# Performance work log

Hardware: AMD Instinct MI355X
Metric: run time of the kernel (lower is better)

## Reference

```python
import jax, jax.numpy as jnp
import numpy as np

BN_EPS = 1e-5

def _bn_train(x, g, b):
    # BatchNorm1d in training mode: biased batch stats over the row dim
    m = x.mean(0)
    v = x.var(0)
    return g * (x - m) * jax.lax.rsqrt(v + BN_EPS) + b


def setup_inputs() -> dict:
    key = jax.random.key(0)
    ks = jax.random.split(key, 16)
    N, V, C, H, T, NC, OD, EH, EC = 128, 128, 256, 512, 12, 5, 5, 256, 256
    s = 0.05
    idx = jax.random.randint(ks[1], (T, N), 0, NC)
    return {
        "x": jax.random.normal(ks[0], (N, V, C), jnp.float32),
        "hidden_states": jnp.zeros((N, V, H), jnp.float32),
        "cell_states": jnp.zeros((N, V, H), jnp.float32),
        "one_hots_c_pred_seq": jax.nn.one_hot(idx, NC, dtype=jnp.float32),
        "W_ih": jax.random.normal(ks[2], (4 * H, C), jnp.float32) * s,
        "W_hh": jax.random.normal(ks[3], (4 * H, H), jnp.float32) * s,
        "b_ih": jax.random.normal(ks[4], (4 * H,), jnp.float32) * s,
        "b_hh": jax.random.normal(ks[5], (4 * H,), jnp.float32) * s,
        "W_cls": jax.random.normal(ks[6], (NC, H), jnp.float32) * s,
        "b_cls": jax.random.normal(ks[7], (NC,), jnp.float32) * s,
        "W_eh": jax.random.normal(ks[8], (EH, H), jnp.float32) * s,
        "b_eh": jax.random.normal(ks[9], (EH,), jnp.float32) * s,
        "g_eh": jnp.ones((EH,), jnp.float32),
        "beta_eh": jnp.zeros((EH,), jnp.float32),
        "W_ec": jax.random.normal(ks[10], (EC, NC), jnp.float32) * s,
        "b_ec": jax.random.normal(ks[11], (EC,), jnp.float32) * s,
        "g_ec": jnp.ones((EC,), jnp.float32),
        "beta_ec": jnp.zeros((EC,), jnp.float32),
        "W_out": jax.random.normal(ks[12], (OD, EH + EC), jnp.float32) * s,
        "b_out": jax.random.normal(ks[13], (OD,), jnp.float32) * s,
    }


def reference(x, hidden_states, cell_states, one_hots_c_pred_seq,
              W_ih, W_hh, b_ih, b_hh, W_cls, b_cls,
              W_eh, b_eh, g_eh, beta_eh, W_ec, b_ec, g_ec, beta_ec,
              W_out, b_out):
    N, V, C = x.shape
    H = hidden_states.shape[-1]
    xf = x.reshape(N * V, C)
    gx = xf @ W_ih.T + b_ih  # input gates are identical every step (x is repeated)

    def step(carry, onehot):
        h, c = carry  # [N*V, H]
        gates = gx + h @ W_hh.T + b_hh
        i, f, g, o = jnp.split(gates, 4, axis=1)  # pytorch LSTMCell gate order
        c = jax.nn.sigmoid(f) * c + jax.nn.sigmoid(i) * jnp.tanh(g)
        h = jax.nn.sigmoid(o) * jnp.tanh(c)
        # ClassifierLayer: avg-pool over V then 1x1 conv == mean + linear
        oc = h.reshape(N, V, H).mean(1) @ W_cls.T + b_cls  # [N, nc]
        # PredictionLayer
        eh = jax.nn.relu(_bn_train(h @ W_eh.T + b_eh, g_eh, beta_eh))
        ohr = jnp.broadcast_to(onehot[:, None, :], (N, V, onehot.shape[-1])).reshape(N * V, -1)
        ec = jax.nn.relu(_bn_train(ohr @ W_ec.T + b_ec, g_ec, beta_ec))
        op = jnp.concatenate([eh, ec], axis=1) @ W_out.T + b_out  # [N*V, out_dim]
        return (h, c), (op.reshape(N, V, -1), oc)

    carry0 = (hidden_states.reshape(N * V, H), cell_states.reshape(N * V, H))
    _, (preds, c_outs) = jax.lax.scan(step, carry0, one_hots_c_pred_seq)
    preds = preds.transpose(1, 0, 2, 3)  # [N, T, V, out_dim]
    # output_activation: bivariate-Gaussian params
    pred_outs = jnp.stack([preds[..., 0], preds[..., 1],
                           jnp.exp(preds[..., 2]), jnp.exp(preds[..., 3]),
                           jnp.tanh(preds[..., 4])], axis=-1)
    return pred_outs, c_outs
```

## Files before the change

kernel.cpp:

```cpp
#include <hip/hip_runtime.h>
#include <hip/hip_bf16.h>
#include <stdint.h>

typedef __hip_bfloat16 bf16;
typedef __attribute__((ext_vector_type(8))) short bf16x8;
typedef __attribute__((ext_vector_type(4))) short bf16x4;
typedef __attribute__((ext_vector_type(4))) float f32x4;

#define NN 128
#define VV 128
#define CC 256
#define HH 512
#define TT 12
#define NCLS 5
#define OD 5
#define EHD 256
#define KCAT (HH + CC)
#define ROWS (NN * VV)
#define PRED_SZ (NN * TT * VV * OD)
#define LDP 72
#define MiB (1ull << 20)


__device__ __forceinline__ float sigm(float x) { return 1.f / (1.f + __expf(-x)); }
__device__ __forceinline__ float tanh_(float x) {
    x = fminf(fmaxf(x, -15.f), 15.f);
    float e = __expf(2.f * x);
    return (e - 1.f) / (e + 1.f);
}
__device__ __forceinline__ float bf2f(unsigned short v) {
    unsigned u = ((unsigned)v) << 16; float f; __builtin_memcpy(&f, &u, 4); return f;
}
__device__ __forceinline__ float ldin(const void* p, int i, int is32) {
    return is32 ? ((const float*)p)[i] : __bfloat162float(((const bf16*)p)[i]);
}

__global__ void detect_dtype(const void* g_eh, int* flag, int* hnz) {
    unsigned w = *(const unsigned*)g_eh;
    *flag = (w == 0x3F800000u) ? 1 : 0;
    *hnz = 0;
}

__global__ __launch_bounds__(256) void convert_in(const void* src, bf16* dst, int n, const int* flag) {
    int is32 = *flag;
    int i = blockIdx.x * 256 + threadIdx.x;
    int stride = gridDim.x * 256;
    if (is32) { const float* s = (const float*)src; for (; i < n; i += stride) dst[i] = __float2bfloat16(s[i]); }
    else      { const bf16*  s = (const bf16*)src;  for (; i < n; i += stride) dst[i] = s[i]; }
}

__global__ __launch_bounds__(256) void convert_in_hflag(const void* src, bf16* dst, int n, const int* flag,
                                                        int* nz) {
    int is32 = *flag;
    int i = blockIdx.x * 256 + threadIdx.x;
    int stride = gridDim.x * 256;
    int loc = 0;
    if (is32) {
        const float* s = (const float*)src;
        for (; i < n; i += stride) { float v = s[i]; if (__float_as_uint(v) != 0u) loc = 1; dst[i] = __float2bfloat16(v); }
    } else {
        const bf16* s = (const bf16*)src;
        for (; i < n; i += stride) { bf16 v = s[i]; if (*(const unsigned short*)&v) loc = 1; dst[i] = v; }
    }
    if (loc) atomicOr(nz, 1);
}

__global__ __launch_bounds__(256) void init_c(const void* cell, bf16* c, const int* flag) {
    int is32 = *flag;
    size_t i = (size_t)blockIdx.x * 256 + threadIdx.x;
    const size_t total = (size_t)ROWS * HH;
    for (; i < total; i += (size_t)8192 * 256) c[i] = __float2bfloat16(ldin(cell, (int)i, is32));
}

__device__ __forceinline__ void issue_loads(const bf16* __restrict__ A, int lda, int row0, int ka,
                                            const bf16* __restrict__ B, int ldb, int col0, int kb,
                                            bf16x8 ar[4], bf16x8 br[4]) {
    int tid = threadIdx.x;
#pragma unroll
    for (int it = 0; it < 4; ++it) {
        int cidx = tid + 256 * it;
        int row = cidx >> 3;
        int cc8 = (cidx & 7) * 8;
        ar[it] = *(const bf16x8*)(A + (size_t)(row0 + row) * lda + ka + cc8);
        br[it] = *(const bf16x8*)(B + (size_t)(col0 + row) * ldb + kb + cc8);
    }
}
__device__ __forceinline__ void write_lds(bf16* As, bf16* Bs, const bf16x8 ar[4], const bf16x8 br[4]) {
    int tid = threadIdx.x;
#pragma unroll
    for (int it = 0; it < 4; ++it) {
        int cidx = tid + 256 * it;
        int row = cidx >> 3;
        int cc8 = (cidx & 7) * 8;
        *(bf16x8*)(As + row * LDP + cc8) = ar[it];
        *(bf16x8*)(Bs + row * LDP + cc8) = br[it];
    }
}

__device__ __forceinline__ void tile_mfma(const bf16* As, const bf16* Bs, f32x4 acc[4][4]) {
    const int lane = threadIdx.x & 63, wave = threadIdx.x >> 6;
    const int wro = (wave >> 1) * 64, wco = (wave & 1) * 64;
    const int l15 = lane & 15, l8 = (lane >> 4) * 8;
#pragma unroll
    for (int kk = 0; kk < 64; kk += 32) {
        bf16x8 af[4], bg[4];
#pragma unroll
        for (int x = 0; x < 4; ++x) {
            af[x] = *(const bf16x8*)(As + (wro + x * 16 + l15) * LDP + kk + l8);
            bg[x] = *(const bf16x8*)(Bs + (wco + x * 16 + l15) * LDP + kk + l8);
        }
#pragma unroll
        for (int bi = 0; bi < 4; ++bi)
#pragma unroll
            for (int bj = 0; bj < 4; ++bj)
                acc[bi][bj] = __builtin_amdgcn_mfma_f32_16x16x32_bf16(af[bi], bg[bj], acc[bi][bj], 0, 0, 0);
    }
}

__global__ __launch_bounds__(256) void prep_weights(const void* __restrict__ Wih, const void* __restrict__ Whh,
                                                    const void* __restrict__ bih, const void* __restrict__ bhh,
                                                    bf16* __restrict__ Wihp, bf16* __restrict__ Whhp,
                                                    float* __restrict__ biasp, const int* flag) {
    int is32 = *flag;
    int jg = blockIdx.x;
    int b = jg >> 7, j = jg & 127;
    int gate = (j >> 4) & 3;
    int unit = b * 32 + (j & 15) + 16 * (j >> 6);
    int p = gate * HH + unit;
    for (int k = threadIdx.x; k < HH; k += 256)
        Whhp[(size_t)jg * HH + k] = __float2bfloat16(ldin(Whh, p * HH + k, is32));
    for (int k = threadIdx.x; k < CC; k += 256)
        Wihp[(size_t)jg * CC + k] = __float2bfloat16(ldin(Wih, p * CC + k, is32));
    if (threadIdx.x == 0)
        biasp[jg] = ldin(bih, p, is32) + ldin(bhh, p, is32);
}

__global__ __launch_bounds__(256) void gemm_k0(const bf16* __restrict__ A, const bf16* __restrict__ B,
                                               const float* __restrict__ biasp, bf16* __restrict__ gx) {
    __shared__ bf16 As[128 * LDP], Bs[128 * LDP];
    f32x4 acc[4][4] = {};
    bf16x8 ar[4], br[4];
    int row0 = blockIdx.x * 128, col0 = blockIdx.y * 128;
    issue_loads(A, CC, row0, 0, B, CC, col0, 0, ar, br);
    for (int k0 = 0; k0 < CC; k0 += 64) {
        __syncthreads();
        write_lds(As, Bs, ar, br);
        __syncthreads();
        int kn = k0 + 64;
        if (kn < CC) issue_loads(A, CC, row0, kn, B, CC, col0, kn, ar, br);
        tile_mfma(As, Bs, acc);
    }
    int lane = threadIdx.x & 63, wave = threadIdx.x >> 6;
    int wro = (wave >> 1) * 64, wco = (wave & 1) * 64;
    int l15 = lane & 15, lr4 = (lane >> 4) * 4;
#pragma unroll
    for (int bj = 0; bj < 4; ++bj) {
        int j = wco + bj * 16 + l15;
        float bia = biasp[col0 + j];
        int sidx = wco + l15 * 4 + bj;
#pragma unroll
        for (int bi = 0; bi < 4; ++bi)
#pragma unroll
            for (int reg = 0; reg < 4; ++reg) {
                int r = row0 + wro + bi * 16 + lr4 + reg;
                gx[(size_t)r * 2048 + col0 + sidx] = __float2bfloat16(acc[bi][bj][reg] + bia);
            }
    }
}

__global__ __launch_bounds__(256) void ec_precompute(const void* __restrict__ W_ec, const void* __restrict__ b_ec,
                                                     const void* __restrict__ g_ec, const void* __restrict__ beta_ec,
                                                     const void* __restrict__ W_out, const void* __restrict__ b_out,
                                                     const void* __restrict__ onehot, float* __restrict__ ecd_all,
                                                     const int* flag) {
    __shared__ float ecv[NCLS][EHD];
    __shared__ float cntf[NCLS];
    __shared__ float ecdc[NCLS][OD];
    int is32 = *flag;
    int t = blockIdx.x, tid = threadIdx.x;
    int ohoff = t * NN * NCLS;
    if (tid < NCLS) {
        float cnum = 0.f;
        for (int n = 0; n < NN; ++n) cnum += ldin(onehot, ohoff + n * NCLS + tid, is32);
        cntf[tid] = cnum * (1.f / NN);
    }
    __syncthreads();
    {
        int j = tid;
        float vals[NCLS];
        float m = 0.f, e2 = 0.f;
        float be = ldin(b_ec, j, is32);
        for (int cc = 0; cc < NCLS; ++cc) {
            vals[cc] = ldin(W_ec, j * NCLS + cc, is32) + be;
            m += cntf[cc] * vals[cc];
            e2 += cntf[cc] * vals[cc] * vals[cc];
        }
        float rs = rsqrtf(e2 - m * m + 1e-5f);
        float g = ldin(g_ec, j, is32), bt = ldin(beta_ec, j, is32);
        for (int cc = 0; cc < NCLS; ++cc)
            ecv[cc][j] = fmaxf(g * (vals[cc] - m) * rs + bt, 0.f);
    }
    __syncthreads();
    if (tid < NCLS * OD) {
        int cc = tid / OD, k = tid % OD;
        float s = 0.f;
        for (int j = 0; j < EHD; ++j) s += ecv[cc][j] * ldin(W_out, k * (EHD * 2) + EHD + j, is32);
        ecdc[cc][k] = s;
    }
    __syncthreads();
    if (tid < NN) {
        for (int k = 0; k < OD; ++k) {
            float s = ldin(b_out, k, is32);
            for (int cc = 0; cc < NCLS; ++cc) s += ldin(onehot, ohoff + tid * NCLS + cc, is32) * ecdc[cc][k];
            ecd_all[((size_t)t * NN + tid) * OD + k] = s;
        }
    }
}

__global__ __launch_bounds__(256) void lstm_gemm_gx(const bf16* __restrict__ h_in, const bf16* __restrict__ Whhp,
                                                    const bf16* __restrict__ gx, bf16* __restrict__ c,
                                                    bf16* __restrict__ h_out, float* __restrict__ csum,
                                                    float* __restrict__ colsum, float* __restrict__ colss) {
    __shared__ bf16 As[128 * LDP], Bs[128 * LDP];
    __shared__ float hsum[32];
    f32x4 acc[4][4] = {};
    bf16x8 ar[4], br[4];
    bf16x4 gpre[16];
    unsigned short cpre[16];
    int row0 = blockIdx.x * 128, col0 = blockIdx.y * 128;
    int tid = threadIdx.x, lane = tid & 63, wave = tid >> 6;
    int wro = (wave >> 1) * 64;
    int l15 = lane & 15, lr4 = (lane >> 4) * 4;
    int ul = (wave & 1) * 16 + l15;
    int u = blockIdx.y * 32 + ul;
    const bf16* gxp = gx + col0 + (wave & 1) * 64 + l15 * 4;
    issue_loads(h_in, HH, row0, 0, Whhp, HH, col0, 0, ar, br);
#pragma unroll
    for (int k0 = 0; k0 < HH; k0 += 64) {
        __syncthreads();
        write_lds(As, Bs, ar, br);
        __syncthreads();
        int kn = k0 + 64;
        if (kn < HH) issue_loads(h_in, HH, row0, kn, Whhp, HH, col0, kn, ar, br);
#pragma unroll
        for (int e = 0; e < 2; ++e) {
            int idx = (k0 >> 6) * 2 + e;
            int bi = idx >> 2, reg = idx & 3;
            int r = row0 + wro + bi * 16 + lr4 + reg;
            gpre[idx] = *(const bf16x4*)(gxp + (size_t)r * 2048);
            cpre[idx] = *(const unsigned short*)(c + (size_t)r * HH + u);
        }
        tile_mfma(As, Bs, acc);
    }
    if (tid < 32) hsum[tid] = 0.f;
    if (blockIdx.x == 0 && blockIdx.y == 0) { colsum[tid & 255] = 0.f; colss[tid & 255] = 0.f; }
    __syncthreads();
    float hpart = 0.f;
#pragma unroll
    for (int bi = 0; bi < 4; ++bi) {
#pragma unroll
        for (int reg = 0; reg < 4; ++reg) {
            int idx = bi * 4 + reg;
            int r = row0 + wro + bi * 16 + lr4 + reg;
            float gi = acc[bi][0][reg] + bf2f((unsigned short)gpre[idx][0]);
            float gf = acc[bi][1][reg] + bf2f((unsigned short)gpre[idx][1]);
            float gg = acc[bi][2][reg] + bf2f((unsigned short)gpre[idx][2]);
            float go = acc[bi][3][reg] + bf2f((unsigned short)gpre[idx][3]);
            float iv = sigm(gi), fv = sigm(gf), gv = tanh_(gg), ov = sigm(go);
            size_t ci = (size_t)r * HH + u;
            float cn = fv * bf2f(cpre[idx]) + iv * gv;
            c[ci] = __float2bfloat16(cn);
            float hv = ov * tanh_(cn);
            h_out[ci] = __float2bfloat16(hv);
            hpart += hv;
        }
    }
    atomicAdd(&hsum[ul], hpart);
    __syncthreads();
    if (tid < 32) csum[(size_t)blockIdx.x * HH + blockIdx.y * 32 + tid] = hsum[tid];
}

__global__ __launch_bounds__(256) void lstm_gemm_gx_first(const bf16* __restrict__ h_in, const bf16* __restrict__ Whhp,
                                                          const bf16* __restrict__ gx, bf16* __restrict__ c,
                                                          bf16* __restrict__ h_out, float* __restrict__ csum,
                                                          float* __restrict__ colsum, float* __restrict__ colss,
                                                          const int* __restrict__ gemm_flag) {
    __shared__ bf16 As[128 * LDP], Bs[128 * LDP];
    __shared__ float hsum[32];
    f32x4 acc[4][4] = {};
    bf16x8 ar[4], br[4];
    bf16x4 gpre[16];
    unsigned short cpre[16];
    int row0 = blockIdx.x * 128, col0 = blockIdx.y * 128;
    int tid = threadIdx.x, lane = tid & 63, wave = tid >> 6;
    int wro = (wave >> 1) * 64;
    int l15 = lane & 15, lr4 = (lane >> 4) * 4;
    int ul = (wave & 1) * 16 + l15;
    int u = blockIdx.y * 32 + ul;
    const bf16* gxp = gx + col0 + (wave & 1) * 64 + l15 * 4;
    const int do_gemm = *gemm_flag;
    if (do_gemm) {
        issue_loads(h_in, HH, row0, 0, Whhp, HH, col0, 0, ar, br);
#pragma unroll
        for (int k0 = 0; k0 < HH; k0 += 64) {
            __syncthreads();
            write_lds(As, Bs, ar, br);
            __syncthreads();
            int kn = k0 + 64;
            if (kn < HH) issue_loads(h_in, HH, row0, kn, Whhp, HH, col0, kn, ar, br);
#pragma unroll
            for (int e = 0; e < 2; ++e) {
                int idx = (k0 >> 6) * 2 + e;
                int bi = idx >> 2, reg = idx & 3;
                int r = row0 + wro + bi * 16 + lr4 + reg;
                gpre[idx] = *(const bf16x4*)(gxp + (size_t)r * 2048);
                cpre[idx] = *(const unsigned short*)(c + (size_t)r * HH + u);
            }
            tile_mfma(As, Bs, acc);
        }
    } else {
#pragma unroll
        for (int idx = 0; idx < 16; ++idx) {
            int bi = idx >> 2, reg = idx & 3;
            int r = row0 + wro + bi * 16 + lr4 + reg;
            gpre[idx] = *(const bf16x4*)(gxp + (size_t)r * 2048);
            cpre[idx] = *(const unsigned short*)(c + (size_t)r * HH + u);
        }
    }
    if (tid < 32) hsum[tid] = 0.f;
    if (blockIdx.x == 0 && blockIdx.y == 0) { colsum[tid & 255] = 0.f; colss[tid & 255] = 0.f; }
    __syncthreads();
    float hpart = 0.f;
#pragma unroll
    for (int bi = 0; bi < 4; ++bi) {
#pragma unroll
        for (int reg = 0; reg < 4; ++reg) {
            int idx = bi * 4 + reg;
            int r = row0 + wro + bi * 16 + lr4 + reg;
            float gi = acc[bi][0][reg] + bf2f((unsigned short)gpre[idx][0]);
            float gf = acc[bi][1][reg] + bf2f((unsigned short)gpre[idx][1]);
            float gg = acc[bi][2][reg] + bf2f((unsigned short)gpre[idx][2]);
            float go = acc[bi][3][reg] + bf2f((unsigned short)gpre[idx][3]);
            float iv = sigm(gi), fv = sigm(gf), gv = tanh_(gg), ov = sigm(go);
            size_t ci = (size_t)r * HH + u;
            float cn = fv * bf2f(cpre[idx]) + iv * gv;
            c[ci] = __float2bfloat16(cn);
            float hv = ov * tanh_(cn);
            h_out[ci] = __float2bfloat16(hv);
            hpart += hv;
        }
    }
    atomicAdd(&hsum[ul], hpart);
    __syncthreads();
    if (tid < 32) csum[(size_t)blockIdx.x * HH + blockIdx.y * 32 + tid] = hsum[tid];
}

__global__ __launch_bounds__(256) void lstm_gemm_cat(const bf16* __restrict__ h_in, const bf16* __restrict__ x,
                                                     const bf16* __restrict__ Wihp, const bf16* __restrict__ Whhp,
                                                     const float* __restrict__ biasp, bf16* __restrict__ c,
                                                     bf16* __restrict__ h_out, float* __restrict__ csum,
                                                     float* __restrict__ colsum, float* __restrict__ colss) {
    __shared__ bf16 As[128 * LDP], Bs[128 * LDP];
    __shared__ float hsum[32];
    f32x4 acc[4][4] = {};
    bf16x8 ar[4], br[4];
    int row0 = blockIdx.x * 128, col0 = blockIdx.y * 128;
    issue_loads(h_in, HH, row0, 0, Whhp, HH, col0, 0, ar, br);
    for (int k0 = 0; k0 < KCAT; k0 += 64) {
        __syncthreads();
        write_lds(As, Bs, ar, br);
        __syncthreads();
        int kn = k0 + 64;
        if (kn < KCAT) {
            if (kn < HH) issue_loads(h_in, HH, row0, kn, Whhp, HH, col0, kn, ar, br);
            else         issue_loads(x, CC, row0, kn - HH, Wihp, CC, col0, kn - HH, ar, br);
        }
        tile_mfma(As, Bs, acc);
    }
    int tid = threadIdx.x;
    if (tid < 32) hsum[tid] = 0.f;
    if (blockIdx.x == 0 && blockIdx.y == 0) { colsum[tid & 255] = 0.f; colss[tid & 255] = 0.f; }
    __syncthreads();
    int lane = tid & 63, wave = tid >> 6;
    int wro = (wave >> 1) * 64;
    int l15 = lane & 15, lr4 = (lane >> 4) * 4;
    int ul = (wave & 1) * 16 + l15;
    int u = blockIdx.y * 32 + ul;
    int colp = col0 + (wave & 1) * 64 + l15;
    float b0 = biasp[colp], b1 = biasp[colp + 16], b2 = biasp[colp + 32], b3 = biasp[colp + 48];
    float hpart = 0.f;
#pragma unroll
    for (int bi = 0; bi < 4; ++bi) {
#pragma unroll
        for (int reg = 0; reg < 4; ++reg) {
            int r = row0 + wro + bi * 16 + lr4 + reg;
            float gi = acc[bi][0][reg] + b0;
            float gf = acc[bi][1][reg] + b1;
            float gg = acc[bi][2][reg] + b2;
            float go = acc[bi][3][reg] + b3;
            float iv = sigm(gi), fv = sigm(gf), gv = tanh_(gg), ov = sigm(go);
            size_t ci = (size_t)r * HH + u;
            float cn = fv * __bfloat162float(c[ci]) + iv * gv;
            c[ci] = __float2bfloat16(cn);
            float hv = ov * tanh_(cn);
            h_out[ci] = __float2bfloat16(hv);
            hpart += hv;
        }
    }
    atomicAdd(&hsum[ul], hpart);
    __syncthreads();
    if (tid < 32) csum[(size_t)blockIdx.x * HH + blockIdx.y * 32 + tid] = hsum[tid];
}

__device__ __forceinline__ void final_rows(int grp, const bf16* __restrict__ ehp, const float* __restrict__ colsum,
                                           const float* __restrict__ colss, const void* __restrict__ g_eh,
                                           const void* __restrict__ beta_eh, const float* __restrict__ ecd_all,
                                           const float* Wl, void* __restrict__ out, int t, int is32) {
    int wave = threadIdx.x >> 6, lane = threadIdx.x & 63;
    int r = grp * 4 + wave;
    int j0 = lane * 4;
    float av[4], bv[4];
#pragma unroll
    for (int e = 0; e < 4; ++e) {
        float mean = colsum[j0 + e] * (1.f / ROWS);
        float var = colss[j0 + e] * (1.f / ROWS) - mean * mean;
        float a = ldin(g_eh, j0 + e, is32) * rsqrtf(var + 1e-5f);
        av[e] = a;
        bv[e] = ldin(beta_eh, j0 + e, is32) - mean * a;
    }
    bf16x4 xs = *(const bf16x4*)(ehp + (size_t)r * EHD + j0);
    float v0 = fmaxf(av[0] * bf2f((unsigned short)xs[0]) + bv[0], 0.f);
    float v1 = fmaxf(av[1] * bf2f((unsigned short)xs[1]) + bv[1], 0.f);
    float v2 = fmaxf(av[2] * bf2f((unsigned short)xs[2]) + bv[2], 0.f);
    float v3 = fmaxf(av[3] * bf2f((unsigned short)xs[3]) + bv[3], 0.f);
    float p[OD];
#pragma unroll
    for (int k = 0; k < OD; ++k)
        p[k] = v0 * Wl[k * EHD + j0] + v1 * Wl[k * EHD + j0 + 1] + v2 * Wl[k * EHD + j0 + 2] + v3 * Wl[k * EHD + j0 + 3];
#pragma unroll
    for (int off = 32; off; off >>= 1)
#pragma unroll
        for (int k = 0; k < OD; ++k) p[k] += __shfl_down(p[k], off, 64);
    if (lane == 0) {
        int n = r >> 7, v = r & 127;
        const float* en = ecd_all + ((size_t)t * NN + n) * OD;
        float o0 = p[0] + en[0];
        float o1 = p[1] + en[1];
        float o2 = expf(p[2] + en[2]);
        float o3 = expf(p[3] + en[3]);
        float o4 = tanh_(p[4] + en[4]);
        size_t base = (size_t)n * (TT * VV * OD) + (size_t)t * (VV * OD) + (size_t)v * OD;
        if (is32) {
            float* dst = (float*)out + base;
            dst[0] = o0; dst[1] = o1; dst[2] = o2; dst[3] = o3; dst[4] = o4;
        } else {
            bf16* dst = (bf16*)out + base;
            dst[0] = __float2bfloat16(o0);
            dst[1] = __float2bfloat16(o1);
            dst[2] = __float2bfloat16(o2);
            dst[3] = __float2bfloat16(o3);
            dst[4] = __float2bfloat16(o4);
        }
    }
}

__global__ __launch_bounds__(256) void eh_cls(const bf16* __restrict__ A, const bf16* __restrict__ B,
                                              const void* __restrict__ bias, bf16* __restrict__ out,
                                              float* __restrict__ colsum, float* __restrict__ colss,
                                              const float* __restrict__ csum, const void* __restrict__ W_cls,
                                              const void* __restrict__ b_cls, void* __restrict__ outp,
                                              int t, const int* flag,
                                              const bf16* __restrict__ ehp_prev, const float* __restrict__ colsum_prev,
                                              const float* __restrict__ colss_prev, const void* __restrict__ g_eh,
                                              const void* __restrict__ beta_eh, const void* __restrict__ W_out,
                                              const float* __restrict__ ecd_all, int tprev) {
    int is32 = *flag;
    int tid = threadIdx.x;
    if (blockIdx.x >= 640) {
        if (tprev < 0) return;
        __shared__ float Wl[OD * EHD];
        for (int i = tid; i < OD * EHD; i += 256)
            Wl[i] = ldin(W_out, (i >> 8) * (EHD * 2) + (i & 255), is32);
        __syncthreads();
        int b = blockIdx.x - 640;
#pragma unroll
        for (int g = 0; g < 4; ++g)
            final_rows(b * 4 + g, ehp_prev, colsum_prev, colss_prev, g_eh, beta_eh,
                       ecd_all, Wl, outp, tprev, is32);
        return;
    }
    if (blockIdx.x >= 512) {
        __shared__ float wl[NCLS * HH];
        __shared__ float wred[4][NCLS];
        int wave = tid >> 6, lane = tid & 63;
        for (int i = tid; i < NCLS * HH; i += 256) wl[i] = ldin(W_cls, i, is32);
        __syncthreads();
        int n = blockIdx.x - 512;
        float pk[NCLS] = {};
        for (int u = tid; u < HH; u += 256) {
            float cv = csum[(size_t)n * HH + u];
#pragma unroll
            for (int k = 0; k < NCLS; ++k) pk[k] += cv * wl[k * HH + u];
        }
#pragma unroll
        for (int off = 32; off; off >>= 1)
#pragma unroll
            for (int k = 0; k < NCLS; ++k) pk[k] += __shfl_down(pk[k], off, 64);
        if (lane == 0)
#pragma unroll
            for (int k = 0; k < NCLS; ++k) wred[wave][k] = pk[k];
        __syncthreads();
        if (tid < NCLS) {
            float a = (wred[0][tid] + wred[1][tid] + wred[2][tid] + wred[3][tid]) * (1.f / VV) + ldin(b_cls, tid, is32);
            int idx = PRED_SZ + t * (NN * NCLS) + n * NCLS + tid;
            if (is32) ((float*)outp)[idx] = a;
            else      ((bf16*)outp)[idx] = __float2bfloat16(a);
        }
        return;
    }
    __shared__ bf16 As[64 * LDP], Bs[128 * LDP];
    __shared__ float s_sum[128], s_ss[128];
    f32x4 acc[4][2] = {};
    bf16x8 ar[2], br[4];
    int row0 = (blockIdx.x >> 1) * 64, col0 = (blockIdx.x & 1) * 128;
#pragma unroll
    for (int it = 0; it < 2; ++it) { int cx = tid + 256 * it; ar[it] = *(const bf16x8*)(A + (size_t)(row0 + (cx >> 3)) * HH + (cx & 7) * 8); }
#pragma unroll
    for (int it = 0; it < 4; ++it) { int cx = tid + 256 * it; br[it] = *(const bf16x8*)(B + (size_t)(col0 + (cx >> 3)) * HH + (cx & 7) * 8); }
    const int lane = tid & 63, wave = tid >> 6;
    const int l15 = lane & 15, l8 = (lane >> 4) * 8;
    for (int k0 = 0; k0 < HH; k0 += 64) {
        __syncthreads();
#pragma unroll
        for (int it = 0; it < 2; ++it) { int cx = tid + 256 * it; *(bf16x8*)(As + (cx >> 3) * LDP + (cx & 7) * 8) = ar[it]; }
#pragma unroll
        for (int it = 0; it < 4; ++it) { int cx = tid + 256 * it; *(bf16x8*)(Bs + (cx >> 3) * LDP + (cx & 7) * 8) = br[it]; }
        __syncthreads();
        int kn = k0 + 64;
        if (kn < HH) {
#pragma unroll
            for (int it = 0; it < 2; ++it) { int cx = tid + 256 * it; ar[it] = *(const bf16x8*)(A + (size_t)(row0 + (cx >> 3)) * HH + kn + (cx & 7) * 8); }
#pragma unroll
            for (int it = 0; it < 4; ++it) { int cx = tid + 256 * it; br[it] = *(const bf16x8*)(B + (size_t)(col0 + (cx >> 3)) * HH + kn + (cx & 7) * 8); }
        }
#pragma unroll
        for (int kk = 0; kk < 64; kk += 32) {
            bf16x8 af[4], bg[2];
#pragma unroll
            for (int x = 0; x < 4; ++x) af[x] = *(const bf16x8*)(As + (x * 16 + l15) * LDP + kk + l8);
#pragma unroll
            for (int x = 0; x < 2; ++x) bg[x] = *(const bf16x8*)(Bs + (wave * 32 + x * 16 + l15) * LDP + kk + l8);
#pragma unroll
            for (int bi = 0; bi < 4; ++bi)
#pragma unroll
                for (int bj = 0; bj < 2; ++bj)
                    acc[bi][bj] = __builtin_amdgcn_mfma_f32_16x16x32_bf16(af[bi], bg[bj], acc[bi][bj], 0, 0, 0);
        }
    }
    int lr4 = (lane >> 4) * 4;
    if (tid < 128) { s_sum[tid] = 0.f; s_ss[tid] = 0.f; }
    __syncthreads();
#pragma unroll
    for (int bj = 0; bj < 2; ++bj) {
        int j = wave * 32 + bj * 16 + l15;
        int col = col0 + j;
        float bia = ldin(bias, col, is32);
        float ps = 0.f, pss = 0.f;
#pragma unroll
        for (int bi = 0; bi < 4; ++bi)
#pragma unroll
            for (int reg = 0; reg < 4; ++reg) {
                int r = row0 + bi * 16 + lr4 + reg;
                float val = acc[bi][bj][reg] + bia;
                out[(size_t)r * EHD + col] = __float2bfloat16(val);
                ps += val; pss += val * val;
            }
        atomicAdd(&s_sum[j], ps);
        atomicAdd(&s_ss[j], pss);
    }
    __syncthreads();
    if (tid < 128) {
        atomicAdd(&colsum[col0 + tid], s_sum[tid]);
        atomicAdd(&colss[col0 + tid], s_ss[tid]);
    }
}

__global__ __launch_bounds__(256) void final_kernel(const bf16* __restrict__ eh_pre, const float* __restrict__ colsum,
                                                    const float* __restrict__ colss, const void* __restrict__ g_eh,
                                                    const void* __restrict__ beta_eh, const void* __restrict__ W_out,
                                                    const float* __restrict__ ecd_all, void* __restrict__ out,
                                                    int t, const int* flag) {
    __shared__ float Wl[OD * EHD];
    int is32 = *flag;
    for (int i = threadIdx.x; i < OD * EHD; i += 256)
        Wl[i] = ldin(W_out, (i >> 8) * (EHD * 2) + (i & 255), is32);
    __syncthreads();
    final_rows(blockIdx.x, eh_pre, colsum, colss, g_eh, beta_eh, ecd_all, Wl, out, t, is32);
}

extern "C" void kernel_launch(void* const* d_in, const int* in_sizes, int n_in,
                              void* d_out, int out_size, void* d_ws, size_t ws_size,
                              hipStream_t stream) {
    const void* x       = d_in[0];
    const void* hidden  = d_in[1];
    const void* cell    = d_in[2];
    const void* onehot  = d_in[3];
    const void* W_ih    = d_in[4];
    const void* W_hh    = d_in[5];
    const void* b_ih    = d_in[6];
    const void* b_hh    = d_in[7];
    const void* W_cls   = d_in[8];
    const void* b_cls   = d_in[9];
    const void* W_eh    = d_in[10];
    const void* b_eh    = d_in[11];
    const void* g_eh    = d_in[12];
    const void* beta_eh = d_in[13];
    const void* W_ec    = d_in[14];
    const void* b_ec    = d_in[15];
    const void* g_ec    = d_in[16];
    const void* beta_ec = d_in[17];
    const void* W_out   = d_in[18];
    const void* b_out   = d_in[19];

    const int use_gx = (ws_size >= 148 * MiB) ? 1 : 0;

    char* ws = (char*)d_ws;
    bf16*  cbuf = (bf16*)(ws);
    bf16*  h0   = (bf16*)(ws + 32 * MiB);
    bf16*  h1   = (bf16*)(ws + 48 * MiB);
    bf16*  gxb  = (bf16*)(ws + 64 * MiB);
    bf16*  ehp0, *ehp1, *x_c, *Wihp, *Whhp, *Weh_c;
    char*  tail;
    if (use_gx) {
        ehp0  = (bf16*)(ws + 128 * MiB);
        x_c   = (bf16*)(ws + 136 * MiB);
        ehp1  = (bf16*)(ws + 136 * MiB);
        Wihp  = (bf16*)(ws + 144 * MiB);
        Whhp  = (bf16*)(ws + 145 * MiB);
        Weh_c = (bf16*)(ws + 147 * MiB);
        tail  = ws + 147 * MiB + 524288;
    } else {
        ehp0  = (bf16*)(ws + 64 * MiB);
        x_c   = (bf16*)(ws + 72 * MiB);
        ehp1  = (bf16*)(ws + 80 * MiB);
        Wihp  = (bf16*)(ws + 88 * MiB);
        Whhp  = (bf16*)(ws + 89 * MiB);
        Weh_c = (bf16*)(ws + 91 * MiB);
        tail  = ws + 91 * MiB + 524288;
    }
    float* biasp   = (float*)(tail);
    float* colsum0 = (float*)(tail + 8192);
    float* colss0  = (float*)(tail + 9216);
    float* colsum1 = (float*)(tail + 10240);
    float* colss1  = (float*)(tail + 11264);
    int*   dflag   = (int*)  (tail + 16384);
    int*   hnz     = (int*)  (tail + 16388);
    float* csum    = (float*)(tail + 20480);
    float* ecd_all = (float*)(tail + 20480 + 262144);

    bf16*  ehp_b[2]    = { ehp0, ehp1 };
    float* colsum_b[2] = { colsum0, colsum1 };
    float* colss_b[2]  = { colss0, colss1 };

    detect_dtype<<<1, 1, 0, stream>>>(g_eh, dflag, hnz);
    convert_in<<<4096, 256, 0, stream>>>(x, x_c, ROWS * CC, dflag);
    convert_in_hflag<<<4096, 256, 0, stream>>>(hidden, h0, ROWS * HH, dflag, hnz);
    convert_in<<<512, 256, 0, stream>>>(W_eh, Weh_c, EHD * HH, dflag);
    init_c<<<8192, 256, 0, stream>>>(cell, cbuf, dflag);
    prep_weights<<<2048, 256, 0, stream>>>(W_ih, W_hh, b_ih, b_hh, Wihp, Whhp, biasp, dflag);
    ec_precompute<<<TT, 256, 0, stream>>>(W_ec, b_ec, g_ec, beta_ec, W_out, b_out, onehot, ecd_all, dflag);
    if (use_gx)
        gemm_k0<<<dim3(128, 16), 256, 0, stream>>>(x_c, Wihp, biasp, gxb);

    for (int t = 0; t < TT; ++t) {
        const bf16* hin = (t & 1) ? h1 : h0;
        bf16* hout = (t & 1) ? h0 : h1;
        int cur = t & 1, prv = (t - 1) & 1;
        if (use_gx) {
            if (t == 0)
                lstm_gemm_gx_first<<<dim3(128, 16), 256, 0, stream>>>(hin, Whhp, gxb, cbuf, hout, csum,
                                                                      colsum_b[cur], colss_b[cur], hnz);
            else
                lstm_gemm_gx<<<dim3(128, 16), 256, 0, stream>>>(hin, Whhp, gxb, cbuf, hout, csum,
                                                                colsum_b[cur], colss_b[cur]);
        } else {
            lstm_gemm_cat<<<dim3(128, 16), 256, 0, stream>>>(hin, x_c, Wihp, Whhp, biasp, cbuf, hout, csum,
                                                             colsum_b[cur], colss_b[cur]);
        }
        eh_cls<<<1664, 256, 0, stream>>>(hout, Weh_c, b_eh, ehp_b[cur], colsum_b[cur], colss_b[cur],
                                         csum, W_cls, b_cls, d_out, t, dflag,
                                         ehp_b[prv], colsum_b[prv], colss_b[prv], g_eh, beta_eh,
                                         W_out, ecd_all, t - 1);
    }
    final_kernel<<<4096, 256, 0, stream>>>(ehp_b[(TT - 1) & 1], colsum_b[(TT - 1) & 1], colss_b[(TT - 1) & 1],
                                           g_eh, beta_eh, W_out, ecd_all, d_out, TT - 1, dflag);
}
```

Baseline: 1.251 ms.

## Fuse LSTM step GEMM with previous-step prediction and classifier work in one launch

Replaces the per-step pair of LSTM-gate and eh/cls launches with a single heterogeneous kernel. Its first 2048 blocks compute the current LSTM step, and the remaining blocks run the eh projection and classifier for step t-1 and the final output for step t-2, which is a software pipeline across timesteps. The column statistics move to a triple buffer and csum to a double buffer so the lagged stages can coexist. The aim is to cut launch count and let the small tail work overlap the big GEMM, at the cost of larger shared memory per block and more buffer rotation logic.

Result: no change. 1.228 ms (-1.8%).

```diff
diff --git a/kernel.cpp b/kernel.cpp
--- a/kernel.cpp
+++ b/kernel.cpp
@@ -96,7 +96,6 @@
         *(bf16x8*)(Bs + row * LDP + cc8) = br[it];
     }
 }
-
 __device__ __forceinline__ void tile_mfma(const bf16* As, const bf16* Bs, f32x4 acc[4][4]) {
     const int lane = threadIdx.x & 63, wave = threadIdx.x >> 6;
     const int wro = (wave >> 1) * 64, wco = (wave & 1) * 64;
@@ -217,67 +216,248 @@
     }
 }
 
-__global__ __launch_bounds__(256) void lstm_gemm_gx(const bf16* __restrict__ h_in, const bf16* __restrict__ Whhp,
-                                                    const bf16* __restrict__ gx, bf16* __restrict__ c,
-                                                    bf16* __restrict__ h_out, float* __restrict__ csum,
-                                                    float* __restrict__ colsum, float* __restrict__ colss) {
-    __shared__ bf16 As[128 * LDP], Bs[128 * LDP];
-    __shared__ float hsum[32];
-    f32x4 acc[4][4] = {};
-    bf16x8 ar[4], br[4];
-    bf16x4 gpre[16];
-    unsigned short cpre[16];
-    int row0 = blockIdx.x * 128, col0 = blockIdx.y * 128;
-    int tid = threadIdx.x, lane = tid & 63, wave = tid >> 6;
-    int wro = (wave >> 1) * 64;
-    int l15 = lane & 15, lr4 = (lane >> 4) * 4;
-    int ul = (wave & 1) * 16 + l15;
-    int u = blockIdx.y * 32 + ul;
-    const bf16* gxp = gx + col0 + (wave & 1) * 64 + l15 * 4;
-    issue_loads(h_in, HH, row0, 0, Whhp, HH, col0, 0, ar, br);
-#pragma unroll
+__device__ __forceinline__ void final_rows(int grp, const bf16* __restrict__ ehp, const float* __restrict__ colsum,
+                                           const float* __restrict__ colss, const void* __restrict__ g_eh,
+                                           const void* __restrict__ beta_eh, const float* __restrict__ ecd_all,
+                                           const float* Wl, void* __restrict__ out, int t, int is32) {
+    int wave = threadIdx.x >> 6, lane = threadIdx.x & 63;
+    int r = grp * 4 + wave;
+    int j0 = lane * 4;
+    float av[4], bv[4];
+#pragma unroll
+    for (int e = 0; e < 4; ++e) {
+        float mean = colsum[j0 + e] * (1.f / ROWS);
+        float var = colss[j0 + e] * (1.f / ROWS) - mean * mean;
+        float a = ldin(g_eh, j0 + e, is32) * rsqrtf(var + 1e-5f);
+        av[e] = a;
+        bv[e] = ldin(beta_eh, j0 + e, is32) - mean * a;
+    }
+    bf16x4 xs = *(const bf16x4*)(ehp + (size_t)r * EHD + j0);
+    float v0 = fmaxf(av[0] * bf2f((unsigned short)xs[0]) + bv[0], 0.f);
+    float v1 = fmaxf(av[1] * bf2f((unsigned short)xs[1]) + bv[1], 0.f);
+    float v2 = fmaxf(av[2] * bf2f((unsigned short)xs[2]) + bv[2], 0.f);
+    float v3 = fmaxf(av[3] * bf2f((unsigned short)xs[3]) + bv[3], 0.f);
+    float p[OD];
+#pragma unroll
+    for (int k = 0; k < OD; ++k)
+        p[k] = v0 * Wl[k * EHD + j0] + v1 * Wl[k * EHD + j0 + 1] + v2 * Wl[k * EHD + j0 + 2] + v3 * Wl[k * EHD + j0 + 3];
+#pragma unroll
+    for (int off = 32; off; off >>= 1)
+#pragma unroll
+        for (int k = 0; k < OD; ++k) p[k] += __shfl_down(p[k], off, 64);
+    if (lane == 0) {
+        int n = r >> 7, v = r & 127;
+        const float* en = ecd_all + ((size_t)t * NN + n) * OD;
+        float o0 = p[0] + en[0];
+        float o1 = p[1] + en[1];
+        float o2 = expf(p[2] + en[2]);
+        float o3 = expf(p[3] + en[3]);
+        float o4 = tanh_(p[4] + en[4]);
+        size_t base = (size_t)n * (TT * VV * OD) + (size_t)t * (VV * OD) + (size_t)v * OD;
+        if (is32) {
+            float* dst = (float*)out + base;
+            dst[0] = o0; dst[1] = o1; dst[2] = o2; dst[3] = o3; dst[4] = o4;
+        } else {
+            bf16* dst = (bf16*)out + base;
+            dst[0] = __float2bfloat16(o0);
+            dst[1] = __float2bfloat16(o1);
+            dst[2] = __float2bfloat16(o2);
+            dst[3] = __float2bfloat16(o3);
+            dst[4] = __float2bfloat16(o4);
+        }
+    }
+}
+
+__global__ __launch_bounds__(256) void lstm_fused(const bf16* __restrict__ h_in, const bf16* __restrict__ Whhp,
+                                                  const bf16* __restrict__ gx, bf16* __restrict__ c,
+                                                  bf16* __restrict__ h_out, float* __restrict__ csum_cur,
+                                                  float* __restrict__ colsum_z, float* __restrict__ colss_z,
+                                                  const bf16* __restrict__ Weh, const void* __restrict__ b_eh,
+                                                  bf16* __restrict__ ehp_w, float* __restrict__ colsum_w,
+                                                  float* __restrict__ colss_w, const float* __restrict__ csum_prev,
+                                                  const void* __restrict__ W_cls, const void* __restrict__ b_cls,
+                                                  void* __restrict__ outp, int t_aux,
+                                                  const bf16* __restrict__ ehp_r, const float* __restrict__ colsum_r,
+                                                  const float* __restrict__ colss_r, const void* __restrict__ g_eh,
+                                                  const void* __restrict__ beta_eh, const void* __restrict__ W_out,
+                                                  const float* __restrict__ ecd_all, int t_final,
+                                                  const int* __restrict__ flag) {
+    __shared__ __align__(16) unsigned char smem[37376];
+    int tid = threadIdx.x;
+    if (blockIdx.x < 2048) {
+        bf16* As = (bf16*)smem;
+        bf16* Bs = (bf16*)(smem + 128 * LDP * 2);
+        float* hsum = (float*)(smem + 36864);
+        f32x4 acc[4][4] = {};
+        bf16x8 ar[4], br[4];
+        bf16x4 gpre[16];
+        unsigned short cpre[16];
+        int row0 = (blockIdx.x & 127) * 128, col0 = (blockIdx.x >> 7) * 128;
+        int lane = tid & 63, wave = tid >> 6;
+        int wro = (wave >> 1) * 64;
+        int l15 = lane & 15, lr4 = (lane >> 4) * 4;
+        int ul = (wave & 1) * 16 + l15;
+        int u = (blockIdx.x >> 7) * 32 + ul;
+        const bf16* gxp = gx + col0 + (wave & 1) * 64 + l15 * 4;
+        issue_loads(h_in, HH, row0, 0, Whhp, HH, col0, 0, ar, br);
+#pragma unroll
+        for (int k0 = 0; k0 < HH; k0 += 64) {
+            __syncthreads();
+            write_lds(As, Bs, ar, br);
+            __syncthreads();
+            int kn = k0 + 64;
+            if (kn < HH) issue_loads(h_in, HH, row0, kn, Whhp, HH, col0, kn, ar, br);
+#pragma unroll
+            for (int e = 0; e < 2; ++e) {
+                int idx = (k0 >> 6) * 2 + e;
+                int bi = idx >> 2, reg = idx & 3;
+                int r = row0 + wro + bi * 16 + lr4 + reg;
+                gpre[idx] = *(const bf16x4*)(gxp + (size_t)r * 2048);
+                cpre[idx] = *(const unsigned short*)(c + (size_t)r * HH + u);
+            }
+            tile_mfma(As, Bs, acc);
+        }
+        if (tid < 32) hsum[tid] = 0.f;
+        if (blockIdx.x == 0) { colsum_z[tid] = 0.f; colss_z[tid] = 0.f; }
+        __syncthreads();
+        float hpart = 0.f;
+#pragma unroll
+        for (int bi = 0; bi < 4; ++bi) {
+#pragma unroll
+            for (int reg = 0; reg < 4; ++reg) {
+                int idx = bi * 4 + reg;
+                int r = row0 + wro + bi * 16 + lr4 + reg;
+                float gi = acc[bi][0][reg] + bf2f((unsigned short)gpre[idx][0]);
+                float gf = acc[bi][1][reg] + bf2f((unsigned short)gpre[idx][1]);
+                float gg = acc[bi][2][reg] + bf2f((unsigned short)gpre[idx][2]);
+                float go = acc[bi][3][reg] + bf2f((unsigned short)gpre[idx][3]);
+                float iv = sigm(gi), fv = sigm(gf), gv = tanh_(gg), ov = sigm(go);
+                size_t ci = (size_t)r * HH + u;
+                float cn = fv * bf2f(cpre[idx]) + iv * gv;
+                c[ci] = __float2bfloat16(cn);
+                float hv = ov * tanh_(cn);
+                h_out[ci] = __float2bfloat16(hv);
+                hpart += hv;
+            }
+        }
+        atomicAdd(&hsum[ul], hpart);
+        __syncthreads();
+        if (tid < 32) csum_cur[(size_t)(blockIdx.x & 127) * HH + (blockIdx.x >> 7) * 32 + tid] = hsum[tid];
+        return;
+    }
+    int is32 = *flag;
+    int b = blockIdx.x - 2048;
+    if (b >= 640) {
+        if (t_final < 0) return;
+        float* Wl = (float*)smem;
+        for (int i = tid; i < OD * EHD; i += 256)
+            Wl[i] = ldin(W_out, (i >> 8) * (EHD * 2) + (i & 255), is32);
+        __syncthreads();
+        int fb = b - 640;
+#pragma unroll
+        for (int g = 0; g < 4; ++g)
+            final_rows(fb * 4 + g, ehp_r, colsum_r, colss_r, g_eh, beta_eh, ecd_all, Wl, outp, t_final, is32);
+        return;
+    }
+    if (b >= 512) {
+        if (t_aux < 0) return;
+        float* wl = (float*)smem;
+        float* wred = (float*)(smem + 10240);
+        int wave = tid >> 6, lane = tid & 63;
+        for (int i = tid; i < NCLS * HH; i += 256) wl[i] = ldin(W_cls, i, is32);
+        __syncthreads();
+        int n = b - 512;
+        float pk[NCLS] = {};
+        for (int u = tid; u < HH; u += 256) {
+            float cv = csum_prev[(size_t)n * HH + u];
+#pragma unroll
+            for (int k = 0; k < NCLS; ++k) pk[k] += cv * wl[k * HH + u];
+        }
+#pragma unroll
+        for (int off = 32; off; off >>= 1)
+#pragma unroll
+            for (int k = 0; k < NCLS; ++k) pk[k] += __shfl_down(pk[k], off, 64);
+        if (lane == 0)
+#pragma unroll
+            for (int k = 0; k < NCLS; ++k) wred[wave * NCLS + k] = pk[k];
+        __syncthreads();
+        if (tid < NCLS) {
+            float a = (wred[tid] + wred[NCLS + tid] + wred[2 * NCLS + tid] + wred[3 * NCLS + tid]) * (1.f / VV)
+                      + ldin(b_cls, tid, is32);
+            int idx = PRED_SZ + t_aux * (NN * NCLS) + n * NCLS + tid;
+            if (is32) ((float*)outp)[idx] = a;
+            else      ((bf16*)outp)[idx] = __float2bfloat16(a);
+        }
+        return;
+    }
+    if (t_aux < 0) return;
+    bf16* As = (bf16*)smem;
+    bf16* Bs = (bf16*)(smem + 9216);
+    float* s_sum = (float*)(smem + 27648);
+    float* s_ss  = (float*)(smem + 28160);
+    f32x4 acc[4][2] = {};
+    bf16x8 ar[2], br[4];
+    int row0 = (b >> 1) * 64, col0 = (b & 1) * 128;
+#pragma unroll
+    for (int it = 0; it < 2; ++it) { int cx = tid + 256 * it; ar[it] = *(const bf16x8*)(h_in + (size_t)(row0 + (cx >> 3)) * HH + (cx & 7) * 8); }
+#pragma unroll
+    for (int it = 0; it < 4; ++it) { int cx = tid + 256 * it; br[it] = *(const bf16x8*)(Weh + (size_t)(col0 + (cx >> 3)) * HH + (cx & 7) * 8); }
+    const int lane = tid & 63, wave = tid >> 6;
+    const int l15 = lane & 15, l8 = (lane >> 4) * 8;
     for (int k0 = 0; k0 < HH; k0 += 64) {
         __syncthreads();
-        write_lds(As, Bs, ar, br);
+#pragma unroll
+        for (int it = 0; it < 2; ++it) { int cx = tid + 256 * it; *(bf16x8*)(As + (cx >> 3) * LDP + (cx & 7) * 8) = ar[it]; }
+#pragma unroll
+        for (int it = 0; it < 4; ++it) { int cx = tid + 256 * it; *(bf16x8*)(Bs + (cx >> 3) * LDP + (cx & 7) * 8) = br[it]; }
         __syncthreads();
         int kn = k0 + 64;
-        if (kn < HH) issue_loads(h_in, HH, row0, kn, Whhp, HH, col0, kn, ar, br);
-#pragma unroll
-        for (int e = 0; e < 2; ++e) {
-            int idx = (k0 >> 6) * 2 + e;
-            int bi = idx >> 2, reg = idx & 3;
-            int r = row0 + wro + bi * 16 + lr4 + reg;
-            gpre[idx] = *(const bf16x4*)(gxp + (size_t)r * 2048);
-            cpre[idx] = *(const unsigned short*)(c + (size_t)r * HH + u);
-        }
-        tile_mfma(As, Bs, acc);
-    }
-    if (tid < 32) hsum[tid] = 0.f;
-    if (blockIdx.x == 0 && blockIdx.y == 0) { colsum[tid & 255] = 0.f; colss[tid & 255] = 0.f; }
-    __syncthreads();
-    float hpart = 0.f;
-#pragma unroll
-    for (int bi = 0; bi < 4; ++bi) {
-#pragma unroll
-        for (int reg = 0; reg < 4; ++reg) {
-            int idx = bi * 4 + reg;
-            int r = row0 + wro + bi * 16 + lr4 + reg;
-            float gi = acc[bi][0][reg] + bf2f((unsigned short)gpre[idx][0]);
-            float gf = acc[bi][1][reg] + bf2f((unsigned short)gpre[idx][1]);
-            float gg = acc[bi][2][reg] + bf2f((unsigned short)gpre[idx][2]);
-            float go = acc[bi][3][reg] + bf2f((unsigned short)gpre[idx][3]);
-            float iv = sigm(gi), fv = sigm(gf), gv = tanh_(gg), ov = sigm(go);
-            size_t ci = (size_t)r * HH + u;
-            float cn = fv * bf2f(cpre[idx]) + iv * gv;
-            c[ci] = __float2bfloat16(cn);
-            float hv = ov * tanh_(cn);
-            h_out[ci] = __float2bfloat16(hv);
-            hpart += hv;
-        }
-    }
-    atomicAdd(&hsum[ul], hpart);
-    __syncthreads();
-    if (tid < 32) csum[(size_t)blockIdx.x * HH + blockIdx.y * 32 + tid] = hsum[tid];
+        if (kn < HH) {
+#pragma unroll
+            for (int it = 0; it < 2; ++it) { int cx = tid + 256 * it; ar[it] = *(const bf16x8*)(h_in + (size_t)(row0 + (cx >> 3)) * HH + kn + (cx & 7) * 8); }
+#pragma unroll
+            for (int it = 0; it < 4; ++it) { int cx = tid + 256 * it; br[it] = *(const bf16x8*)(Weh + (size_t)(col0 + (cx >> 3)) * HH + kn + (cx & 7) * 8); }
+        }
+#pragma unroll
+        for (int kk = 0; kk < 64; kk += 32) {
+            bf16x8 af[4], bg[2];
+#pragma unroll
+            for (int x = 0; x < 4; ++x) af[x] = *(const bf16x8*)(As + (x * 16 + l15) * LDP + kk + l8);
+#pragma unroll
+            for (int x = 0; x < 2; ++x) bg[x] = *(const bf16x8*)(Bs + (wave * 32 + x * 16 + l15) * LDP + kk + l8);
+#pragma unroll
+            for (int bi = 0; bi < 4; ++bi)
+#pragma unroll
+                for (int bj = 0; bj < 2; ++bj)
+                    acc[bi][bj] = __builtin_amdgcn_mfma_f32_16x16x32_bf16(af[bi], bg[bj], acc[bi][bj], 0, 0, 0);
+        }
+    }
+    int lr4 = (lane >> 4) * 4;
+    if (tid < 128) { s_sum[tid] = 0.f; s_ss[tid] = 0.f; }
+    __syncthreads();
+#pragma unroll
+    for (int bj = 0; bj < 2; ++bj) {
+        int j = wave * 32 + bj * 16 + l15;
+        int col = col0 + j;
+        float bia = ldin(b_eh, col, is32);
+        float ps = 0.f, pss = 0.f;
+#pragma unroll
+        for (int bi = 0; bi < 4; ++bi)
+#pragma unroll
+            for (int reg = 0; reg < 4; ++reg) {
+                int r = row0 + bi * 16 + lr4 + reg;
+                float val = acc[bi][bj][reg] + bia;
+                ehp_w[(size_t)r * EHD + col] = __float2bfloat16(val);
+                ps += val; pss += val * val;
+            }
+        atomicAdd(&s_sum[j], ps);
+        atomicAdd(&s_ss[j], pss);
+    }
+    __syncthreads();
+    if (tid < 128) {
+        atomicAdd(&colsum_w[col0 + tid], s_sum[tid]);
+        atomicAdd(&colss_w[col0 + tid], s_ss[tid]);
+    }
 }
 
 __global__ __launch_bounds__(256) void lstm_gemm_gx_first(const bf16* __restrict__ h_in, const bf16* __restrict__ Whhp,
@@ -328,7 +508,7 @@
         }
     }
     if (tid < 32) hsum[tid] = 0.f;
-    if (blockIdx.x == 0 && blockIdx.y == 0) { colsum[tid & 255] = 0.f; colss[tid & 255] = 0.f; }
+    if (blockIdx.x == 0 && blockIdx.y == 0) { colsum[tid] = 0.f; colss[tid] = 0.f; }
     __syncthreads();
     float hpart = 0.f;
 #pragma unroll
@@ -379,7 +559,7 @@
     }
     int tid = threadIdx.x;
     if (tid < 32) hsum[tid] = 0.f;
-    if (blockIdx.x == 0 && blockIdx.y == 0) { colsum[tid & 255] = 0.f; colss[tid & 255] = 0.f; }
+    if (blockIdx.x == 0 && blockIdx.y == 0) { colsum[tid] = 0.f; colss[tid] = 0.f; }
     __syncthreads();
     int lane = tid & 63, wave = tid >> 6;
     int wro = (wave >> 1) * 64;
@@ -412,58 +592,6 @@
     if (tid < 32) csum[(size_t)blockIdx.x * HH + blockIdx.y * 32 + tid] = hsum[tid];
 }
 
-__device__ __forceinline__ void final_rows(int grp, const bf16* __restrict__ ehp, const float* __restrict__ colsum,
-                                           const float* __restrict__ colss, const void* __restrict__ g_eh,
-                                           const void* __restrict__ beta_eh, const float* __restrict__ ecd_all,
-                                           const float* Wl, void* __restrict__ out, int t, int is32) {
-    int wave = threadIdx.x >> 6, lane = threadIdx.x & 63;
-    int r = grp * 4 + wave;
-    int j0 = lane * 4;
-    float av[4], bv[4];
-#pragma unroll
-    for (int e = 0; e < 4; ++e) {
-        float mean = colsum[j0 + e] * (1.f / ROWS);
-        float var = colss[j0 + e] * (1.f / ROWS) - mean * mean;
-        float a = ldin(g_eh, j0 + e, is32) * rsqrtf(var + 1e-5f);
-        av[e] = a;
-        bv[e] = ldin(beta_eh, j0 + e, is32) - mean * a;
-    }
-    bf16x4 xs = *(const bf16x4*)(ehp + (size_t)r * EHD + j0);
-    float v0 = fmaxf(av[0] * bf2f((unsigned short)xs[0]) + bv[0], 0.f);
-    float v1 = fmaxf(av[1] * bf2f((unsigned short)xs[1]) + bv[1], 0.f);
-    float v2 = fmaxf(av[2] * bf2f((unsigned short)xs[2]) + bv[2], 0.f);
-    float v3 = fmaxf(av[3] * bf2f((unsigned short)xs[3]) + bv[3], 0.f);
-    float p[OD];
-#pragma unroll
-    for (int k = 0; k < OD; ++k)
-        p[k] = v0 * Wl[k * EHD + j0] + v1 * Wl[k * EHD + j0 + 1] + v2 * Wl[k * EHD + j0 + 2] + v3 * Wl[k * EHD + j0 + 3];
-#pragma unroll
-    for (int off = 32; off; off >>= 1)
-#pragma unroll
-        for (int k = 0; k < OD; ++k) p[k] += __shfl_down(p[k], off, 64);
-    if (lane == 0) {
-        int n = r >> 7, v = r & 127;
-        const float* en = ecd_all + ((size_t)t * NN + n) * OD;
-        float o0 = p[0] + en[0];
-        float o1 = p[1] + en[1];
-        float o2 = expf(p[2] + en[2]);
-        float o3 = expf(p[3] + en[3]);
-        float o4 = tanh_(p[4] + en[4]);
-        size_t base = (size_t)n * (TT * VV * OD) + (size_t)t * (VV * OD) + (size_t)v * OD;
-        if (is32) {
-            float* dst = (float*)out + base;
-            dst[0] = o0; dst[1] = o1; dst[2] = o2; dst[3] = o3; dst[4] = o4;
-        } else {
-            bf16* dst = (bf16*)out + base;
-            dst[0] = __float2bfloat16(o0);
-            dst[1] = __float2bfloat16(o1);
-            dst[2] = __float2bfloat16(o2);
-            dst[3] = __float2bfloat16(o3);
-            dst[4] = __float2bfloat16(o4);
-        }
-    }
-}
-
 __global__ __launch_bounds__(256) void eh_cls(const bf16* __restrict__ A, const bf16* __restrict__ B,
                                               const void* __restrict__ bias, bf16* __restrict__ out,
                                               float* __restrict__ colsum, float* __restrict__ colss,
@@ -474,24 +602,25 @@
                                               const float* __restrict__ colss_prev, const void* __restrict__ g_eh,
                                               const void* __restrict__ beta_eh, const void* __restrict__ W_out,
                                               const float* __restrict__ ecd_all, int tprev) {
+    __shared__ __align__(16) unsigned char smem[37376];
     int is32 = *flag;
     int tid = threadIdx.x;
     if (blockIdx.x >= 640) {
         if (tprev < 0) return;
-        __shared__ float Wl[OD * EHD];
+        float* Wl = (float*)smem;
         for (int i = tid; i < OD * EHD; i += 256)
             Wl[i] = ldin(W_out, (i >> 8) * (EHD * 2) + (i & 255), is32);
         __syncthreads();
-        int b = blockIdx.x - 640;
+        int fb = blockIdx.x - 640;
 #pragma unroll
         for (int g = 0; g < 4; ++g)
-            final_rows(b * 4 + g, ehp_prev, colsum_prev, colss_prev, g_eh, beta_eh,
+            final_rows(fb * 4 + g, ehp_prev, colsum_prev, colss_prev, g_eh, beta_eh,
                        ecd_all, Wl, outp, tprev, is32);
         return;
     }
     if (blockIdx.x >= 512) {
-        __shared__ float wl[NCLS * HH];
-        __shared__ float wred[4][NCLS];
+        float* wl = (float*)smem;
+        float* wred = (float*)(smem + 10240);
         int wave = tid >> 6, lane = tid & 63;
         for (int i = tid; i < NCLS * HH; i += 256) wl[i] = ldin(W_cls, i, is32);
         __syncthreads();
@@ -508,18 +637,21 @@
             for (int k = 0; k < NCLS; ++k) pk[k] += __shfl_down(pk[k], off, 64);
         if (lane == 0)
 #pragma unroll
-            for (int k = 0; k < NCLS; ++k) wred[wave][k] = pk[k];
+            for (int k = 0; k < NCLS; ++k) wred[wave * NCLS + k] = pk[k];
         __syncthreads();
         if (tid < NCLS) {
-            float a = (wred[0][tid] + wred[1][tid] + wred[2][tid] + wred[3][tid]) * (1.f / VV) + ldin(b_cls, tid, is32);
+            float a = (wred[tid] + wred[NCLS + tid] + wred[2 * NCLS + tid] + wred[3 * NCLS + tid]) * (1.f / VV)
+                      + ldin(b_cls, tid, is32);
             int idx = PRED_SZ + t * (NN * NCLS) + n * NCLS + tid;
             if (is32) ((float*)outp)[idx] = a;
             else      ((bf16*)outp)[idx] = __float2bfloat16(a);
         }
         return;
     }
-    __shared__ bf16 As[64 * LDP], Bs[128 * LDP];
-    __shared__ float s_sum[128], s_ss[128];
+    bf16* As = (bf16*)smem;
+    bf16* Bs = (bf16*)(smem + 9216);
+    float* s_sum = (float*)(smem + 27648);
+    float* s_ss  = (float*)(smem + 28160);
     f32x4 acc[4][2] = {};
     bf16x8 ar[2], br[4];
     int row0 = (blockIdx.x >> 1) * 64, col0 = (blockIdx.x & 1) * 128;
@@ -626,11 +758,11 @@
 
     char* ws = (char*)d_ws;
     bf16*  cbuf = (bf16*)(ws);
+    char*  tail = ws + 16 * MiB;
     bf16*  h0   = (bf16*)(ws + 32 * MiB);
     bf16*  h1   = (bf16*)(ws + 48 * MiB);
     bf16*  gxb  = (bf16*)(ws + 64 * MiB);
     bf16*  ehp0, *ehp1, *x_c, *Wihp, *Whhp, *Weh_c;
-    char*  tail;
     if (use_gx) {
         ehp0  = (bf16*)(ws + 128 * MiB);
         x_c   = (bf16*)(ws + 136 * MiB);
@@ -638,7 +770,6 @@
         Wihp  = (bf16*)(ws + 144 * MiB);
         Whhp  = (bf16*)(ws + 145 * MiB);
         Weh_c = (bf16*)(ws + 147 * MiB);
-        tail  = ws + 147 * MiB + 524288;
     } else {
         ehp0  = (bf16*)(ws + 64 * MiB);
         x_c   = (bf16*)(ws + 72 * MiB);
@@ -646,21 +777,18 @@
         Wihp  = (bf16*)(ws + 88 * MiB);
         Whhp  = (bf16*)(ws + 89 * MiB);
         Weh_c = (bf16*)(ws + 91 * MiB);
-        tail  = ws + 91 * MiB + 524288;
     }
     float* biasp   = (float*)(tail);
-    float* colsum0 = (float*)(tail + 8192);
-    float* colss0  = (float*)(tail + 9216);
-    float* colsum1 = (float*)(tail + 10240);
-    float* colss1  = (float*)(tail + 11264);
+    float* colsum3[3] = { (float*)(tail + 8192), (float*)(tail + 10240), (float*)(tail + 12288) };
+    float* colss3[3]  = { (float*)(tail + 9216), (float*)(tail + 11264), (float*)(tail + 13312) };
     int*   dflag   = (int*)  (tail + 16384);
     int*   hnz     = (int*)  (tail + 16388);
-    float* csum    = (float*)(tail + 20480);
-    float* ecd_all = (float*)(tail + 20480 + 262144);
-
-    bf16*  ehp_b[2]    = { ehp0, ehp1 };
-    float* colsum_b[2] = { colsum0, colsum1 };
-    float* colss_b[2]  = { colss0, colss1 };
+    float* csum0   = (float*)(tail + 20480);
+    float* csum1   = (float*)(tail + 20480 + 262144);
+    float* ecd_all = (float*)(tail + 20480 + 524288);
+
+    bf16*  ehp_b[2]  = { ehp0, ehp1 };
+    float* csum_b[2] = { csum0, csum1 };
 
     detect_dtype<<<1, 1, 0, stream>>>(g_eh, dflag, hnz);
     convert_in<<<4096, 256, 0, stream>>>(x, x_c, ROWS * CC, dflag);
@@ -672,26 +800,42 @@
     if (use_gx)
         gemm_k0<<<dim3(128, 16), 256, 0, stream>>>(x_c, Wihp, biasp, gxb);
 
-    for (int t = 0; t < TT; ++t) {
-        const bf16* hin = (t & 1) ? h1 : h0;
-        bf16* hout = (t & 1) ? h0 : h1;
-        int cur = t & 1, prv = (t - 1) & 1;
-        if (use_gx) {
-            if (t == 0)
-                lstm_gemm_gx_first<<<dim3(128, 16), 256, 0, stream>>>(hin, Whhp, gxb, cbuf, hout, csum,
-                                                                      colsum_b[cur], colss_b[cur], hnz);
-            else
-                lstm_gemm_gx<<<dim3(128, 16), 256, 0, stream>>>(hin, Whhp, gxb, cbuf, hout, csum,
-                                                                colsum_b[cur], colss_b[cur]);
-        } else {
-            lstm_gemm_cat<<<dim3(128, 16), 256, 0, stream>>>(hin, x_c, Wihp, Whhp, biasp, cbuf, hout, csum,
-                                                             colsum_b[cur], colss_b[cur]);
-        }
-        eh_cls<<<1664, 256, 0, stream>>>(hout, Weh_c, b_eh, ehp_b[cur], colsum_b[cur], colss_b[cur],
-                                         csum, W_cls, b_cls, d_out, t, dflag,
-                                         ehp_b[prv], colsum_b[prv], colss_b[prv], g_eh, beta_eh,
-                                         W_out, ecd_all, t - 1);
-    }
-    final_kernel<<<4096, 256, 0, stream>>>(ehp_b[(TT - 1) & 1], colsum_b[(TT - 1) & 1], colss_b[(TT - 1) & 1],
-                                           g_eh, beta_eh, W_out, ecd_all, d_out, TT - 1, dflag);
-}
+    if (use_gx) {
+        lstm_gemm_gx_first<<<dim3(128, 16), 256, 0, stream>>>(h0, Whhp, gxb, cbuf, h1, csum_b[0],
+                                                              colsum3[0], colss3[0], hnz);
+        for (int t = 1; t < TT; ++t) {
+            const bf16* hin = (t & 1) ? h1 : h0;
+            bf16* hout = (t & 1) ? h0 : h1;
+            int tp = t - 1, tf = t - 2;
+            lstm_fused<<<3712, 256, 0, stream>>>(
+                hin, Whhp, gxb, cbuf, hout, csum_b[t & 1], colsum3[t % 3], colss3[t % 3],
+                Weh_c, b_eh, ehp_b[tp & 1], colsum3[tp % 3], colss3[tp % 3], csum_b[tp & 1],
+                W_cls, b_cls, d_out, tp,
+                ehp_b[t & 1] , colsum3[(tf + 3) % 3], colss3[(tf + 3) % 3],
+                g_eh, beta_eh, W_out, ecd_all, tf, dflag);
+        }
+        {
+            int t = TT - 1;
+            const bf16* h_last = (t & 1) ? h1 : h0;
+            eh_cls<<<1664, 256, 0, stream>>>(h_last, Weh_c, b_eh, ehp_b[t & 1], colsum3[t % 3], colss3[t % 3],
+                                             csum_b[t & 1], W_cls, b_cls, d_out, t, dflag,
+                                             ehp_b[(t - 1) & 1], colsum3[(t - 1) % 3], colss3[(t - 1) % 3],
+                                             g_eh, beta_eh, W_out, ecd_all, t - 1);
+            final_kernel<<<4096, 256, 0, stream>>>(ehp_b[t & 1], colsum3[t % 3], colss3[t % 3],
+                                                   g_eh, beta_eh, W_out, ecd_all, d_out, t, dflag);
+        }
+    } else {
+        for (int t = 0; t < TT; ++t) {
+            const bf16* hin = (t & 1) ? h1 : h0;
+            bf16* hout = (t & 1) ? h0 : h1;
+            lstm_gemm_cat<<<dim3(128, 16), 256, 0, stream>>>(hin, x_c, Wihp, Whhp, biasp, cbuf, hout,
+                                                             csum_b[t & 1], colsum3[t % 3], colss3[t % 3]);
+            eh_cls<<<1664, 256, 0, stream>>>(hout, Weh_c, b_eh, ehp_b[t & 1], colsum3[t % 3], colss3[t % 3],
+                                             csum_b[t & 1], W_cls, b_cls, d_out, t, dflag,
+                                             ehp_b[(t - 1) & 1], colsum3[((t - 1) + 3) % 3], colss3[((t - 1) + 3) % 3],
+                                             g_eh, beta_eh, W_out, ecd_all, t - 1);
+        }
+        final_kernel<<<4096, 256, 0, stream>>>(ehp_b[(TT - 1) & 1], colsum3[(TT - 1) % 3], colss3[(TT - 1) % 3],
+                                               g_eh, beta_eh, W_out, ecd_all, d_out, TT - 1, dflag);
+    }
+}
```
